# Performance work log

Measured on AMD Instinct MI355X. Metric: run time of the kernel, lower is better.

The kernel has to match this reference:

```python
import jax, jax.numpy as jnp
import numpy as np

B, N, C, H = 8, 4096, 768, 8


def setup_inputs() -> dict:
    key = jax.random.key(0)
    k1, k2, k3 = jax.random.split(key, 3)
    x = jax.random.normal(k1, (B, N, C), dtype=jnp.float32)
    W_qkv = jax.random.normal(k2, (C, 3 * C), dtype=jnp.float32) * 0.02
    W_proj = jax.random.normal(k3, (C, C), dtype=jnp.float32) * 0.02
    b_proj = jnp.zeros((C,), dtype=jnp.float32)
    temp = jnp.ones((H, 1, 1), dtype=jnp.float32)
    return {"x": x, "W_qkv": W_qkv, "W_proj": W_proj, "b_proj": b_proj, "temp": temp}


def reference(x, W_qkv, W_proj, b_proj, temp):
    b, n, c = x.shape
    h = temp.shape[0]
    d = c // h
    # qkv: [B,N,3C] -> [B,N,H,D,3]  (matches tf.reshape split order)
    qkv = (x @ W_qkv).reshape(b, n, h, d, 3)
    q, k, v = qkv[..., 0], qkv[..., 1], qkv[..., 2]
    # L2-normalize along the patch axis (axis=1), as tf.linalg.normalize
    q = q / jnp.linalg.norm(q, axis=1, keepdims=True)
    k = k / jnp.linalg.norm(k, axis=1, keepdims=True)
    # channel-wise (cross-covariance) attention: [B,H,D,D]
    attn = jnp.einsum('bnhd,bnhe->bhde', q, k) * temp
    attn = jax.nn.softmax(attn, axis=-1)
    # apply to v and fold heads back: [B,N,C]
    y = jnp.einsum('bhde,bnhe->bnhd', attn, v).reshape(b, n, c)
    return y @ W_proj + b_proj
```

## Files before the change

kernel.cpp:

```cpp
#include <hip/hip_runtime.h>

typedef __attribute__((ext_vector_type(8))) short short8;
typedef __attribute__((ext_vector_type(4))) float f32x4;

__device__ inline unsigned short f2b(float f) {
  unsigned int u = __builtin_bit_cast(unsigned int, f);
  u = (u + 0x7FFFu + ((u >> 16) & 1u)) >> 16;
  return (unsigned short)u;
}
__device__ inline float b2f(unsigned short s) {
  unsigned int u = ((unsigned int)s) << 16;
  return __builtin_bit_cast(float, u);
}

__device__ inline void async16(const void* g, void* l) {
  __builtin_amdgcn_global_load_lds((__attribute__((address_space(1))) void*)(g),
                                   (__attribute__((address_space(3))) void*)(l), 16, 0, 0);
}

__global__ void cvt_x(const float4* __restrict__ x, ushort4* __restrict__ xb, int n4) {
  int i = blockIdx.x * blockDim.x + threadIdx.x;
  int stride = gridDim.x * blockDim.x;
  for (; i < n4; i += stride) {
    float4 v = x[i];
    ushort4 o;
    o.x = f2b(v.x); o.y = f2b(v.y); o.z = f2b(v.z); o.w = f2b(v.w);
    xb[i] = o;
  }
}

__global__ __launch_bounds__(256) void t_wqkv(const float* __restrict__ W, unsigned short* __restrict__ Wt) {
  __shared__ float tile[32][33];
  int j0 = blockIdx.x * 32, c0 = blockIdx.y * 32;
  int tx = threadIdx.x & 31, ty = threadIdx.x >> 5;
#pragma unroll
  for (int r = 0; r < 32; r += 8)
    tile[ty + r][tx] = W[(size_t)(c0 + ty + r) * 2304 + j0 + tx];
  __syncthreads();
#pragma unroll
  for (int r = 0; r < 32; r += 8) {
    int j = j0 + ty + r;
    int h = j / 288, rem = j - h * 288;
    int d = rem / 3, s = rem - d * 3;
    int jj = s * 768 + h * 96 + d;
    Wt[(size_t)jj * 768 + c0 + tx] = f2b(tile[tx][ty + r]);
  }
}

__global__ __launch_bounds__(256) void t_wproj(const float* __restrict__ W, unsigned short* __restrict__ Wt) {
  __shared__ float tile[32][33];
  int j0 = blockIdx.x * 32, c0 = blockIdx.y * 32;
  int tx = threadIdx.x & 31, ty = threadIdx.x >> 5;
#pragma unroll
  for (int r = 0; r < 32; r += 8)
    tile[ty + r][tx] = W[(size_t)(c0 + ty + r) * 768 + j0 + tx];
  __syncthreads();
#pragma unroll
  for (int r = 0; r < 32; r += 8)
    Wt[(size_t)(j0 + ty + r) * 768 + c0 + tx] = f2b(tile[tx][ty + r]);
}

__global__ __launch_bounds__(256) void gemm_qkv(
    const unsigned short* __restrict__ A, const unsigned short* __restrict__ Bt,
    unsigned short* __restrict__ Q, unsigned short* __restrict__ Kd, unsigned short* __restrict__ V) {
  __shared__ __align__(16) unsigned short As[128 * 64];
  __shared__ __align__(16) unsigned short Bs[128 * 64];
  const int tid = threadIdx.x;
  const int wave = tid >> 6, lane = tid & 63;
  const int mlane = lane & 15, quad = lane >> 4;
  const int m0 = blockIdx.x * 128, n0 = blockIdx.y * 128;
  const int wm = (wave >> 1) * 64, wn = (wave & 1) * 64;
  f32x4 acc[4][4] = {};
  for (int k0 = 0; k0 < 768; k0 += 64) {
    __syncthreads();
#pragma unroll
    for (int t = 0; t < 4; ++t) {
      int ebase = t * 256 + (wave << 6);
      int e = ebase + lane;
      int row = e >> 3, c8 = e & 7;
      async16(A + (size_t)(m0 + row) * 768 + k0 + c8 * 8, As + ebase * 8);
      async16(Bt + (size_t)(n0 + row) * 768 + k0 + c8 * 8, Bs + ebase * 8);
    }
    __syncthreads();
#pragma unroll
    for (int kk = 0; kk < 64; kk += 32) {
      short8 a[4], b[4];
#pragma unroll
      for (int f = 0; f < 4; ++f)
        a[f] = *(const short8*)&As[(wm + f * 16 + mlane) * 64 + kk + quad * 8];
#pragma unroll
      for (int f = 0; f < 4; ++f)
        b[f] = *(const short8*)&Bs[(wn + f * 16 + mlane) * 64 + kk + quad * 8];
#pragma unroll
      for (int i = 0; i < 4; ++i)
#pragma unroll
        for (int j = 0; j < 4; ++j)
          acc[i][j] = __builtin_amdgcn_mfma_f32_16x16x32_bf16(a[i], b[j], acc[i][j], 0, 0, 0);
    }
  }
  const int bb = m0 >> 12;
  const int nb = (m0 & 4095) + wm + quad * 4;
#pragma unroll
  for (int fn = 0; fn < 4; ++fn) {
    int jj = n0 + wn + fn * 16 + mlane;
    int s = jj / 768;
    int hd = jj - s * 768;
    int h = hd / 96;
    int d = hd - h * 96;
    unsigned short* dst = (s == 0) ? Q : (s == 1) ? Kd : V;
    size_t colbase = ((size_t)(bb * 8 + h) * 4096) * 96 + d;
#pragma unroll
    for (int fm = 0; fm < 4; ++fm) {
      int n = nb + fm * 16;
#pragma unroll
      for (int r = 0; r < 4; ++r)
        dst[colbase + (size_t)(n + r) * 96] = f2b(acc[fm][fn][r]);
    }
  }
}

__global__ __launch_bounds__(256) void sumsq_qk(
    const unsigned short* __restrict__ Q, const unsigned short* __restrict__ Kd,
    float* __restrict__ sq, float* __restrict__ sk) {
  int bh = blockIdx.x, chunk = blockIdx.y;
  int t = threadIdx.x;
  __shared__ float lq[96], lk[96];
  if (t < 96) { lq[t] = 0.f; lk[t] = 0.f; }
  __syncthreads();
  int c = t % 48, rg = t / 48;
  if (rg < 5) {
    const unsigned int* qp = (const unsigned int*)(Q + (size_t)bh * 4096 * 96);
    const unsigned int* kp = (const unsigned int*)(Kd + (size_t)bh * 4096 * 96);
    int base = chunk * 256;
    float aq0 = 0, aq1 = 0, ak0 = 0, ak1 = 0;
    for (int n = rg; n < 256; n += 5) {
      unsigned int qv = qp[(size_t)(base + n) * 48 + c];
      unsigned int kv = kp[(size_t)(base + n) * 48 + c];
      float q0 = b2f(qv & 0xffff), q1 = b2f(qv >> 16);
      float k0 = b2f(kv & 0xffff), k1 = b2f(kv >> 16);
      aq0 += q0 * q0; aq1 += q1 * q1; ak0 += k0 * k0; ak1 += k1 * k1;
    }
    atomicAdd(&lq[2 * c], aq0); atomicAdd(&lq[2 * c + 1], aq1);
    atomicAdd(&lk[2 * c], ak0); atomicAdd(&lk[2 * c + 1], ak1);
  }
  __syncthreads();
  if (t < 96) {
    atomicAdd(&sq[bh * 96 + t], lq[t]);
    atomicAdd(&sk[bh * 96 + t], lk[t]);
  }
}

__global__ __launch_bounds__(256) void attn_partial(
    const unsigned short* __restrict__ Q, const unsigned short* __restrict__ Kd,
    float* __restrict__ Spart) {
  int chunk = blockIdx.x;
  int bh = blockIdx.y;
  __shared__ __align__(16) unsigned short QT[96 * 72];
  __shared__ __align__(16) unsigned short KT[96 * 72];
  int t = threadIdx.x;
  int wave = t >> 6, lane = t & 63, mlane = lane & 15, quad = lane >> 4;
  int wrow = (wave >> 1) * 48, wcol = (wave & 1) * 48;
  f32x4 acc[3][3] = {};
  const unsigned int* qp = (const unsigned int*)(Q + (size_t)bh * 4096 * 96);
  const unsigned int* kp = (const unsigned int*)(Kd + (size_t)bh * 4096 * 96);
  int c = t % 48, rg = t / 48;
  int nbeg = chunk * 256;
  for (int n0 = nbeg; n0 < nbeg + 256; n0 += 64) {
    __syncthreads();
    if (rg < 5) {
      for (int n = rg; n < 64; n += 5) {
        unsigned int qv = qp[(size_t)(n0 + n) * 48 + c];
        unsigned int kv = kp[(size_t)(n0 + n) * 48 + c];
        QT[(2 * c) * 72 + n] = (unsigned short)(qv & 0xffff);
        QT[(2 * c + 1) * 72 + n] = (unsigned short)(qv >> 16);
        KT[(2 * c) * 72 + n] = (unsigned short)(kv & 0xffff);
        KT[(2 * c + 1) * 72 + n] = (unsigned short)(kv >> 16);
      }
    }
    __syncthreads();
#pragma unroll
    for (int kk = 0; kk < 64; kk += 32) {
      short8 a[3], b[3];
#pragma unroll
      for (int f = 0; f < 3; ++f)
        a[f] = *(const short8*)&QT[(wrow + f * 16 + mlane) * 72 + kk + quad * 8];
#pragma unroll
      for (int f = 0; f < 3; ++f)
        b[f] = *(const short8*)&KT[(wcol + f * 16 + mlane) * 72 + kk + quad * 8];
#pragma unroll
      for (int i = 0; i < 3; ++i)
#pragma unroll
        for (int j = 0; j < 3; ++j)
          acc[i][j] = __builtin_amdgcn_mfma_f32_16x16x32_bf16(a[i], b[j], acc[i][j], 0, 0, 0);
    }
  }
  float* dst = Spart + ((size_t)bh * 16 + chunk) * 9216;
#pragma unroll
  for (int i = 0; i < 3; ++i)
#pragma unroll
    for (int j = 0; j < 3; ++j)
#pragma unroll
      for (int r = 0; r < 4; ++r)
        dst[(wrow + i * 16 + quad * 4 + r) * 96 + wcol + j * 16 + mlane] = acc[i][j][r];
}

__global__ __launch_bounds__(256) void attn_finalize(
    const float* __restrict__ Spart, const float* __restrict__ sq,
    const float* __restrict__ sk, const float* __restrict__ temp,
    unsigned short* __restrict__ P) {
  int bh = blockIdx.x, h = bh & 7;
  __shared__ float S[9216];
  __shared__ float rk[96];
  int t = threadIdx.x;
  const float* base = Spart + (size_t)bh * 16 * 9216;
  for (int i = t; i < 9216; i += 256) {
    float s = 0.f;
#pragma unroll
    for (int c2 = 0; c2 < 16; ++c2) s += base[(size_t)c2 * 9216 + i];
    S[i] = s;
  }
  if (t < 96) rk[t] = rsqrtf(sk[bh * 96 + t]);
  __syncthreads();
  if (t < 96) {
    int d = t;
    float rq = rsqrtf(sq[bh * 96 + d]);
    float tm = temp[h];
    float mx = -1e30f;
    for (int e = 0; e < 96; ++e) {
      float v = S[d * 96 + e] * rq * rk[e] * tm;
      S[d * 96 + e] = v;
      mx = fmaxf(mx, v);
    }
    float sum = 0.f;
    for (int e = 0; e < 96; ++e) {
      float v = expf(S[d * 96 + e] - mx);
      S[d * 96 + e] = v;
      sum += v;
    }
    float inv = 1.0f / sum;
    for (int e = 0; e < 96; ++e)
      P[(size_t)bh * 9216 + d * 96 + e] = f2b(S[d * 96 + e] * inv);
  }
}

__global__ __launch_bounds__(256) void gemm_pv(
    const unsigned short* __restrict__ V, const unsigned short* __restrict__ P,
    unsigned short* __restrict__ y) {
  int bh = blockIdx.y;
  int b = bh >> 3, h = bh & 7;
  int m0 = blockIdx.x * 128;
  int t = threadIdx.x, wave = t >> 6, lane = t & 63, mlane = lane & 15, quad = lane >> 4;
  const unsigned short* Vb = V + (size_t)bh * 4096 * 96;
  const unsigned short* Pb = P + (size_t)bh * 9216;
  f32x4 acc[2][6] = {};
#pragma unroll
  for (int kk = 0; kk < 96; kk += 32) {
    short8 a[2], bfr[6];
#pragma unroll
    for (int i = 0; i < 2; ++i)
      a[i] = *(const short8*)&Vb[(size_t)(m0 + wave * 32 + i * 16 + mlane) * 96 + kk + quad * 8];
#pragma unroll
    for (int j = 0; j < 6; ++j)
      bfr[j] = *(const short8*)&Pb[(j * 16 + mlane) * 96 + kk + quad * 8];
#pragma unroll
    for (int i = 0; i < 2; ++i)
#pragma unroll
      for (int j = 0; j < 6; ++j)
        acc[i][j] = __builtin_amdgcn_mfma_f32_16x16x32_bf16(a[i], bfr[j], acc[i][j], 0, 0, 0);
  }
#pragma unroll
  for (int i = 0; i < 2; ++i) {
    int n = m0 + wave * 32 + i * 16 + quad * 4;
#pragma unroll
    for (int j = 0; j < 6; ++j) {
      int d = j * 16 + mlane;
#pragma unroll
      for (int r = 0; r < 4; ++r)
        y[((size_t)b * 4096 + n + r) * 768 + h * 96 + d] = f2b(acc[i][j][r]);
    }
  }
}

__global__ __launch_bounds__(256) void gemm_proj(
    const unsigned short* __restrict__ A, const unsigned short* __restrict__ Bt,
    const float* __restrict__ bias, float* __restrict__ out) {
  __shared__ __align__(16) unsigned short As[128 * 64];
  __shared__ __align__(16) unsigned short Bs[128 * 64];
  const int tid = threadIdx.x;
  const int wave = tid >> 6, lane = tid & 63;
  const int mlane = lane & 15, quad = lane >> 4;
  const int m0 = blockIdx.x * 128, n0 = blockIdx.y * 128;
  const int wm = (wave >> 1) * 64, wn = (wave & 1) * 64;
  f32x4 acc[4][4] = {};
  for (int k0 = 0; k0 < 768; k0 += 64) {
    __syncthreads();
#pragma unroll
    for (int t = 0; t < 4; ++t) {
      int ebase = t * 256 + (wave << 6);
      int e = ebase + lane;
      int row = e >> 3, c8 = e & 7;
      async16(A + (size_t)(m0 + row) * 768 + k0 + c8 * 8, As + ebase * 8);
      async16(Bt + (size_t)(n0 + row) * 768 + k0 + c8 * 8, Bs + ebase * 8);
    }
    __syncthreads();
#pragma unroll
    for (int kk = 0; kk < 64; kk += 32) {
      short8 a[4], b[4];
#pragma unroll
      for (int f = 0; f < 4; ++f)
        a[f] = *(const short8*)&As[(wm + f * 16 + mlane) * 64 + kk + quad * 8];
#pragma unroll
      for (int f = 0; f < 4; ++f)
        b[f] = *(const short8*)&Bs[(wn + f * 16 + mlane) * 64 + kk + quad * 8];
#pragma unroll
      for (int i = 0; i < 4; ++i)
#pragma unroll
        for (int j = 0; j < 4; ++j)
          acc[i][j] = __builtin_amdgcn_mfma_f32_16x16x32_bf16(a[i], b[j], acc[i][j], 0, 0, 0);
    }
  }
#pragma unroll
  for (int fn = 0; fn < 4; ++fn) {
    int col = n0 + wn + fn * 16 + mlane;
    float bv = bias[col];
#pragma unroll
    for (int fm = 0; fm < 4; ++fm) {
      int m = m0 + wm + fm * 16 + quad * 4;
#pragma unroll
      for (int r = 0; r < 4; ++r)
        out[(size_t)(m + r) * 768 + col] = acc[fm][fn][r] + bv;
    }
  }
}

extern "C" void kernel_launch(void* const* d_in, const int* in_sizes, int n_in,
                              void* d_out, int out_size, void* d_ws, size_t ws_size,
                              hipStream_t stream) {
  const float* x = (const float*)d_in[0];
  const float* Wqkv = (const float*)d_in[1];
  const float* Wproj = (const float*)d_in[2];
  const float* bias = (const float*)d_in[3];
  const float* temp = (const float*)d_in[4];
  float* out = (float*)d_out;

  char* ws = (char*)d_ws;
  size_t off = 0;
  auto alloc = [&](size_t bytes) -> void* {
    void* p = ws + off;
    off += (bytes + 255) & ~(size_t)255;
    return p;
  };
  unsigned short* xb = (unsigned short*)alloc(32768ull * 768 * 2);
  unsigned short* Wtq = (unsigned short*)alloc(2304ull * 768 * 2);
  unsigned short* Wtp = (unsigned short*)alloc(768ull * 768 * 2);
  unsigned short* Q = (unsigned short*)alloc(64ull * 4096 * 96 * 2);
  unsigned short* Kd = (unsigned short*)alloc(64ull * 4096 * 96 * 2);
  unsigned short* V = (unsigned short*)alloc(64ull * 4096 * 96 * 2);
  float* sq = (float*)alloc(64 * 96 * 4);
  float* sk = (float*)alloc(64 * 96 * 4);
  unsigned short* P = (unsigned short*)alloc(64ull * 9216 * 2);
  (void)off; (void)ws_size; (void)in_sizes; (void)n_in; (void)out_size;

  float* Spart = out;

  cvt_x<<<4096, 256, 0, stream>>>((const float4*)x, (ushort4*)xb, 32768 * 768 / 4);
  t_wqkv<<<dim3(72, 24), 256, 0, stream>>>(Wqkv, Wtq);
  t_wproj<<<dim3(24, 24), 256, 0, stream>>>(Wproj, Wtp);
  gemm_qkv<<<dim3(256, 18), 256, 0, stream>>>(xb, Wtq, Q, Kd, V);
  hipMemsetAsync(sq, 0, 64 * 96 * 4, stream);
  hipMemsetAsync(sk, 0, 64 * 96 * 4, stream);
  sumsq_qk<<<dim3(64, 16), 256, 0, stream>>>(Q, Kd, sq, sk);
  attn_partial<<<dim3(16, 64), 256, 0, stream>>>(Q, Kd, Spart);
  attn_finalize<<<64, 256, 0, stream>>>(Spart, sq, sk, temp, P);
  gemm_pv<<<dim3(32, 64), 256, 0, stream>>>(V, P, xb );
  gemm_proj<<<dim3(256, 6), 256, 0, stream>>>(xb , Wtp, bias, out);
}
```

Before: 550.8 us.

## Fuse Q/K sum-of-squares into QKV GEMM epilogue and store Q/K transposed

The QKV GEMM epilogue now writes Q and K in a channel-major [768][B*N] layout with vectorized ushort4 stores. It also computes the per-channel squared norms and accumulates them into sq/sk with atomics, which removes the separate sumsq_qk pass over Q and K. attn_partial then loads contiguous 16-byte vectors straight into its transposed LDS tiles instead of doing scattered 4-byte loads with per-element LDS writes. The trade-off is more global atomics and a second layout path in the GEMM epilogue. The norms are now taken from the fp32 accumulators rather than the bf16-rounded values.

New measurement: 665.5 us. 1.21x slower.

```diff
diff --git a/kernel.cpp b/kernel.cpp
--- a/kernel.cpp
+++ b/kernel.cpp
@@ -62,7 +62,8 @@
 
 __global__ __launch_bounds__(256) void gemm_qkv(
     const unsigned short* __restrict__ A, const unsigned short* __restrict__ Bt,
-    unsigned short* __restrict__ Q, unsigned short* __restrict__ Kd, unsigned short* __restrict__ V) {
+    unsigned short* __restrict__ Qt, unsigned short* __restrict__ Kt, unsigned short* __restrict__ V,
+    float* __restrict__ sq, float* __restrict__ sk) {
   __shared__ __align__(16) unsigned short As[128 * 64];
   __shared__ __align__(16) unsigned short Bs[128 * 64];
   const int tid = threadIdx.x;
@@ -99,99 +100,95 @@
     }
   }
   const int bb = m0 >> 12;
-  const int nb = (m0 & 4095) + wm + quad * 4;
-#pragma unroll
-  for (int fn = 0; fn < 4; ++fn) {
-    int jj = n0 + wn + fn * 16 + mlane;
-    int s = jj / 768;
-    int hd = jj - s * 768;
-    int h = hd / 96;
-    int d = hd - h * 96;
-    unsigned short* dst = (s == 0) ? Q : (s == 1) ? Kd : V;
-    size_t colbase = ((size_t)(bb * 8 + h) * 4096) * 96 + d;
-#pragma unroll
-    for (int fm = 0; fm < 4; ++fm) {
-      int n = nb + fm * 16;
-#pragma unroll
-      for (int r = 0; r < 4; ++r)
-        dst[colbase + (size_t)(n + r) * 96] = f2b(acc[fm][fn][r]);
-    }
-  }
-}
-
-__global__ __launch_bounds__(256) void sumsq_qk(
-    const unsigned short* __restrict__ Q, const unsigned short* __restrict__ Kd,
-    float* __restrict__ sq, float* __restrict__ sk) {
-  int bh = blockIdx.x, chunk = blockIdx.y;
-  int t = threadIdx.x;
-  __shared__ float lq[96], lk[96];
-  if (t < 96) { lq[t] = 0.f; lk[t] = 0.f; }
-  __syncthreads();
-  int c = t % 48, rg = t / 48;
-  if (rg < 5) {
-    const unsigned int* qp = (const unsigned int*)(Q + (size_t)bh * 4096 * 96);
-    const unsigned int* kp = (const unsigned int*)(Kd + (size_t)bh * 4096 * 96);
-    int base = chunk * 256;
-    float aq0 = 0, aq1 = 0, ak0 = 0, ak1 = 0;
-    for (int n = rg; n < 256; n += 5) {
-      unsigned int qv = qp[(size_t)(base + n) * 48 + c];
-      unsigned int kv = kp[(size_t)(base + n) * 48 + c];
-      float q0 = b2f(qv & 0xffff), q1 = b2f(qv >> 16);
-      float k0 = b2f(kv & 0xffff), k1 = b2f(kv >> 16);
-      aq0 += q0 * q0; aq1 += q1 * q1; ak0 += k0 * k0; ak1 += k1 * k1;
-    }
-    atomicAdd(&lq[2 * c], aq0); atomicAdd(&lq[2 * c + 1], aq1);
-    atomicAdd(&lk[2 * c], ak0); atomicAdd(&lk[2 * c + 1], ak1);
-  }
-  __syncthreads();
-  if (t < 96) {
-    atomicAdd(&sq[bh * 96 + t], lq[t]);
-    atomicAdd(&sk[bh * 96 + t], lk[t]);
+  const int s = n0 / 768;
+  if (s < 2) {
+    unsigned short* dst = (s == 0) ? Qt : Kt;
+    float* ss = (s == 0) ? sq : sk;
+#pragma unroll
+    for (int fn = 0; fn < 4; ++fn) {
+      int qrow = (n0 - s * 768) + wn + fn * 16 + mlane;
+      size_t rowbase = (size_t)qrow * 32768;
+      float ssq = 0.f;
+#pragma unroll
+      for (int fm = 0; fm < 4; ++fm) {
+        int m = m0 + wm + fm * 16 + quad * 4;
+        ushort4 o;
+        o.x = f2b(acc[fm][fn][0]);
+        o.y = f2b(acc[fm][fn][1]);
+        o.z = f2b(acc[fm][fn][2]);
+        o.w = f2b(acc[fm][fn][3]);
+        *(ushort4*)(dst + rowbase + m) = o;
+#pragma unroll
+        for (int r = 0; r < 4; ++r) ssq += acc[fm][fn][r] * acc[fm][fn][r];
+      }
+      ssq += __shfl_xor(ssq, 16);
+      ssq += __shfl_xor(ssq, 32);
+      if (quad == 0) {
+        int h = qrow / 96, d = qrow - h * 96;
+        atomicAdd(&ss[(bb * 8 + h) * 96 + d], ssq);
+      }
+    }
+  } else {
+    const int nb = (m0 & 4095) + wm + quad * 4;
+#pragma unroll
+    for (int fn = 0; fn < 4; ++fn) {
+      int jj = n0 + wn + fn * 16 + mlane;
+      int hd = jj - 1536;
+      int h = hd / 96;
+      int d = hd - h * 96;
+      size_t colbase = ((size_t)(bb * 8 + h) * 4096) * 96 + d;
+#pragma unroll
+      for (int fm = 0; fm < 4; ++fm) {
+        int n = nb + fm * 16;
+#pragma unroll
+        for (int r = 0; r < 4; ++r)
+          V[colbase + (size_t)(n + r) * 96] = f2b(acc[fm][fn][r]);
+      }
+    }
   }
 }
 
 __global__ __launch_bounds__(256) void attn_partial(
-    const unsigned short* __restrict__ Q, const unsigned short* __restrict__ Kd,
+    const unsigned short* __restrict__ Qt, const unsigned short* __restrict__ Kt,
     float* __restrict__ Spart) {
   int chunk = blockIdx.x;
   int bh = blockIdx.y;
+  int b = bh >> 3, h = bh & 7;
   __shared__ __align__(16) unsigned short QT[96 * 72];
   __shared__ __align__(16) unsigned short KT[96 * 72];
   int t = threadIdx.x;
   int wave = t >> 6, lane = t & 63, mlane = lane & 15, quad = lane >> 4;
   int wrow = (wave >> 1) * 48, wcol = (wave & 1) * 48;
   f32x4 acc[3][3] = {};
-  const unsigned int* qp = (const unsigned int*)(Q + (size_t)bh * 4096 * 96);
-  const unsigned int* kp = (const unsigned int*)(Kd + (size_t)bh * 4096 * 96);
-  int c = t % 48, rg = t / 48;
+  const unsigned short* qp = Qt + (size_t)h * 96 * 32768 + (size_t)b * 4096;
+  const unsigned short* kp = Kt + (size_t)h * 96 * 32768 + (size_t)b * 4096;
   int nbeg = chunk * 256;
   for (int n0 = nbeg; n0 < nbeg + 256; n0 += 64) {
     __syncthreads();
-    if (rg < 5) {
-      for (int n = rg; n < 64; n += 5) {
-        unsigned int qv = qp[(size_t)(n0 + n) * 48 + c];
-        unsigned int kv = kp[(size_t)(n0 + n) * 48 + c];
-        QT[(2 * c) * 72 + n] = (unsigned short)(qv & 0xffff);
-        QT[(2 * c + 1) * 72 + n] = (unsigned short)(qv >> 16);
-        KT[(2 * c) * 72 + n] = (unsigned short)(kv & 0xffff);
-        KT[(2 * c + 1) * 72 + n] = (unsigned short)(kv >> 16);
-      }
+#pragma unroll
+    for (int it = 0; it < 3; ++it) {
+      int e = it * 256 + t;
+      int d = e >> 3, nn = (e & 7) * 8;
+      short8 v = *(const short8*)(qp + (size_t)d * 32768 + n0 + nn);
+      short8 w = *(const short8*)(kp + (size_t)d * 32768 + n0 + nn);
+      *(short8*)&QT[d * 72 + nn] = v;
+      *(short8*)&KT[d * 72 + nn] = w;
     }
     __syncthreads();
 #pragma unroll
     for (int kk = 0; kk < 64; kk += 32) {
-      short8 a[3], b[3];
+      short8 a[3], bf[3];
 #pragma unroll
       for (int f = 0; f < 3; ++f)
         a[f] = *(const short8*)&QT[(wrow + f * 16 + mlane) * 72 + kk + quad * 8];
 #pragma unroll
       for (int f = 0; f < 3; ++f)
-        b[f] = *(const short8*)&KT[(wcol + f * 16 + mlane) * 72 + kk + quad * 8];
+        bf[f] = *(const short8*)&KT[(wcol + f * 16 + mlane) * 72 + kk + quad * 8];
 #pragma unroll
       for (int i = 0; i < 3; ++i)
 #pragma unroll
         for (int j = 0; j < 3; ++j)
-          acc[i][j] = __builtin_amdgcn_mfma_f32_16x16x32_bf16(a[i], b[j], acc[i][j], 0, 0, 0);
+          acc[i][j] = __builtin_amdgcn_mfma_f32_16x16x32_bf16(a[i], bf[j], acc[i][j], 0, 0, 0);
     }
   }
   float* dst = Spart + ((size_t)bh * 16 + chunk) * 9216;
@@ -353,8 +350,8 @@
   unsigned short* xb = (unsigned short*)alloc(32768ull * 768 * 2);
   unsigned short* Wtq = (unsigned short*)alloc(2304ull * 768 * 2);
   unsigned short* Wtp = (unsigned short*)alloc(768ull * 768 * 2);
-  unsigned short* Q = (unsigned short*)alloc(64ull * 4096 * 96 * 2);
-  unsigned short* Kd = (unsigned short*)alloc(64ull * 4096 * 96 * 2);
+  unsigned short* Qt = (unsigned short*)alloc(768ull * 32768 * 2);
+  unsigned short* Kt = (unsigned short*)alloc(768ull * 32768 * 2);
   unsigned short* V = (unsigned short*)alloc(64ull * 4096 * 96 * 2);
   float* sq = (float*)alloc(64 * 96 * 4);
   float* sk = (float*)alloc(64 * 96 * 4);
@@ -366,11 +363,10 @@
   cvt_x<<<4096, 256, 0, stream>>>((const float4*)x, (ushort4*)xb, 32768 * 768 / 4);
   t_wqkv<<<dim3(72, 24), 256, 0, stream>>>(Wqkv, Wtq);
   t_wproj<<<dim3(24, 24), 256, 0, stream>>>(Wproj, Wtp);
-  gemm_qkv<<<dim3(256, 18), 256, 0, stream>>>(xb, Wtq, Q, Kd, V);
   hipMemsetAsync(sq, 0, 64 * 96 * 4, stream);
   hipMemsetAsync(sk, 0, 64 * 96 * 4, stream);
-  sumsq_qk<<<dim3(64, 16), 256, 0, stream>>>(Q, Kd, sq, sk);
-  attn_partial<<<dim3(16, 64), 256, 0, stream>>>(Q, Kd, Spart);
+  gemm_qkv<<<dim3(256, 18), 256, 0, stream>>>(xb, Wtq, Qt, Kt, V, sq, sk);
+  attn_partial<<<dim3(16, 64), 256, 0, stream>>>(Qt, Kt, Spart);
   attn_finalize<<<64, 256, 0, stream>>>(Spart, sq, sk, temp, P);
   gemm_pv<<<dim3(32, 64), 256, 0, stream>>>(V, P, xb );
   gemm_proj<<<dim3(256, 6), 256, 0, stream>>>(xb , Wtp, bias, out);
```
